# Kernel tuning notes

Hardware: AMD Instinct MI355X
Metric: run time of the kernel (lower is better)

## Reference

```python
import jax, jax.numpy as jnp
import numpy as np

NUM_HEADS = 4
EPS = 1e-5

def _proj(x, W, b):
    # 1x1x1 Conv3d == channel-wise linear: x [B,C,H,W,D], W [Cout,Cin], b [Cout]
    return jnp.einsum('oc,bchwd->bohwd', W, x) + b[None, :, None, None, None]

def setup_inputs() -> dict:
    key = jax.random.key(0)
    ks = jax.random.split(key, 12)
    B, C, H, W, D = 2, 128, 16, 16, 16
    s = 1.0 / np.sqrt(C)
    inp = {
        'query_features': jax.random.normal(ks[0], (B, C, H, W, D), jnp.float32),
        'key_value_features': jax.random.normal(ks[1], (B, C, H, W, D), jnp.float32),
        'Wq': jax.random.normal(ks[2], (C, C), jnp.float32) * s,
        'bq': jax.random.normal(ks[3], (C,), jnp.float32) * 0.01,
        'Wk': jax.random.normal(ks[4], (C, C), jnp.float32) * s,
        'bk': jax.random.normal(ks[5], (C,), jnp.float32) * 0.01,
        'Wv': jax.random.normal(ks[6], (C, C), jnp.float32) * s,
        'bv': jax.random.normal(ks[7], (C,), jnp.float32) * 0.01,
        'Wo': jax.random.normal(ks[8], (C, C), jnp.float32) * s,
        'bo': jax.random.normal(ks[9], (C,), jnp.float32) * 0.01,
    }
    return inp

def reference(query_features, key_value_features, Wq, bq, Wk, bk, Wv, bv, Wo, bo):
    B, C, H, W, D = query_features.shape
    hd = C // NUM_HEADS  # head_dim
    N = H * W * D
    Q = _proj(query_features, Wq, bq).reshape(B, NUM_HEADS, hd, N)
    K = _proj(key_value_features, Wk, bk).reshape(B, NUM_HEADS, hd, N)
    V = _proj(key_value_features, Wv, bv).reshape(B, NUM_HEADS, hd, N)
    scale = hd ** -0.5
    attn = jnp.einsum('bhdn,bhdm->bhnm', Q, K) * scale  # [B,h,N,N]
    attn = jax.nn.softmax(attn, axis=-1)
    out = jnp.einsum('bhnm,bhdm->bhdn', attn, V).reshape(B, C, H, W, D)
    out = _proj(out, Wo, bo)
    res = query_features + out
    # InstanceNorm3d (affine=False): normalize over spatial dims per (B,C)
    mu = jnp.mean(res, axis=(2, 3, 4), keepdims=True)
    var = jnp.var(res, axis=(2, 3, 4), keepdims=True)
    return (res - mu) * jax.lax.rsqrt(var + EPS)
```

## Files before the change

### kernel.cpp

```cpp
#include <hip/hip_runtime.h>
#include <hip/hip_bf16.h>

typedef unsigned short u16;
typedef unsigned int u32;
typedef __bf16 bf16_t;
typedef bf16_t bf16x8 __attribute__((ext_vector_type(8)));
typedef float f32x4 __attribute__((ext_vector_type(4)));

#define NTOT 4096
#define CCH 128
#define QSCL 0.25503486703f

__device__ __forceinline__ float bf2f(u16 x) {
    return __uint_as_float(((u32)x) << 16);
}
__device__ __forceinline__ u32 pkbf(float a, float b) {
    __hip_bfloat162 h = __float22bfloat162_rn(make_float2(a, b));
    u32 r; __builtin_memcpy(&r, &h, 4); return r;
}
__device__ __forceinline__ u16 f2bf(float a) {
    return (u16)(pkbf(a, a) & 0xffffu);
}

__global__ __launch_bounds__(256) void prep_kernel(
    const float* __restrict__ Wq, const float* __restrict__ Wk,
    const float* __restrict__ Wv, const float* __restrict__ Wo,
    const float* __restrict__ bq,
    u16* __restrict__ Wqb, u16* __restrict__ Wkb,
    u16* __restrict__ Wvb, u16* __restrict__ Wob,
    float* __restrict__ bqs)
{
    const int idx = blockIdx.x * 256 + threadIdx.x;
    const int m = idx >> 13;
    const int e = idx & 8191;
    const float* src = (m == 0) ? Wq : (m == 1) ? Wk : (m == 2) ? Wv : Wo;
    u32* dst = (u32*)((m == 0) ? Wqb : (m == 1) ? Wkb : (m == 2) ? Wvb : Wob);
    const float s = (m == 0) ? QSCL : 1.0f;
    float2 f = ((const float2*)src)[e];
    dst[e] = pkbf(f.x * s, f.y * s);
    if (idx < CCH) bqs[idx] = bq[idx] * QSCL;
}

__global__ __launch_bounds__(256, 4) void proj_kernel(
    const float* __restrict__ xq, const float* __restrict__ xkv,
    const u16* __restrict__ Wqb, const float* __restrict__ bqs,
    const u16* __restrict__ Wkb, const float* __restrict__ bk_,
    const u16* __restrict__ Wvb, const float* __restrict__ bv_,
    u16* __restrict__ Qt, u16* __restrict__ Kt, u16* __restrict__ Vn)
{
    const int nt = blockIdx.x, p = blockIdx.y, b = blockIdx.z;
    const float* X    = (p == 0) ? xq : xkv;
    const u16*   Wb   = (p == 0) ? Wqb : (p == 1) ? Wkb : Wvb;
    const float* bias = (p == 0) ? bqs : (p == 1) ? bk_ : bv_;
    const int n0 = nt * 64;
    const int tid = threadIdx.x;

    __shared__ u16 Xt[64 * 128];
    __shared__ u16 Wl[128 * 136];

    #pragma unroll
    for (int k = 0; k < 4; ++k) {
        int n = tid & 63;
        int c = (tid >> 6) + k * 4;
        float f[8];
        #pragma unroll
        for (int j = 0; j < 8; ++j)
            f[j] = X[((size_t)(b * CCH) + 8 * c + j) * NTOT + n0 + n];
        uint4 vv = {pkbf(f[0], f[1]), pkbf(f[2], f[3]), pkbf(f[4], f[5]), pkbf(f[6], f[7])};
        *(uint4*)(Xt + n * 128 + ((c ^ (n & 7)) * 8)) = vv;
    }
    #pragma unroll
    for (int k = 0; k < 8; ++k) {
        int id = tid + k * 256;
        int row = id >> 4;
        int off = (id & 15) * 8;
        *(uint4*)(Wl + row * 136 + off) = *(const uint4*)(Wb + row * 128 + off);
    }
    __syncthreads();

    const int wave = tid >> 6, lane = tid & 63;
    const int quad = lane >> 4, l16 = lane & 15;
    f32x4 acc[8];
    #pragma unroll
    for (int cf = 0; cf < 8; ++cf) acc[cf] = (f32x4){0.f, 0.f, 0.f, 0.f};

    #pragma unroll
    for (int kk = 0; kk < 4; ++kk) {
        bf16x8 bx = *(const bf16x8*)(Xt + (wave * 16 + l16) * 128 +
                                     (((kk * 4 + quad) ^ (l16 & 7)) * 8));
        #pragma unroll
        for (int cf = 0; cf < 8; ++cf) {
            bf16x8 aw = *(const bf16x8*)(Wl + (cf * 16 + l16) * 136 + kk * 32 + quad * 8);
            acc[cf] = __builtin_amdgcn_mfma_f32_16x16x32_bf16(aw, bx, acc[cf], 0, 0, 0);
        }
    }

    const int n = n0 + wave * 16 + l16;
    #pragma unroll
    for (int cf = 0; cf < 8; ++cf) {
        float4 b4 = *(const float4*)(bias + cf * 16 + quad * 4);
        float v0 = acc[cf][0] + b4.x;
        float v1 = acc[cf][1] + b4.y;
        float v2 = acc[cf][2] + b4.z;
        float v3 = acc[cf][3] + b4.w;
        if (p < 2) {
            const int h = cf >> 1;
            const int d0 = (cf & 1) * 16 + quad * 4;
            u16* dst = (p == 0 ? Qt : Kt) + ((size_t)(b * 4 + h) * NTOT + n) * 32 + d0;
            uint2 vv = {pkbf(v0, v1), pkbf(v2, v3)};
            *(uint2*)dst = vv;
        } else {
            int c = cf * 16 + quad * 4;
            u16* dst = Vn + (size_t)(b * CCH + c) * NTOT + n;
            dst[0 * NTOT] = f2bf(v0); dst[1 * NTOT] = f2bf(v1);
            dst[2 * NTOT] = f2bf(v2); dst[3 * NTOT] = f2bf(v3);
        }
    }
}

__global__ __launch_bounds__(256, 2) void flash_attn_kernel(
    const u16* __restrict__ Qt, const u16* __restrict__ Kt,
    const u16* __restrict__ Vn, u16* __restrict__ pO, float* __restrict__ pL)
{
    const int bh = blockIdx.z, kc = blockIdx.y;
    const int wave = threadIdx.x >> 6, lane = threadIdx.x & 63;
    const int q = lane >> 4, l16 = lane & 15;
    const int q0w = blockIdx.x * 256 + wave * 64;

    const u16* Qbh = Qt + (size_t)bh * NTOT * 32;
    const u16* Kbh = Kt + (size_t)bh * NTOT * 32;
    const u16* Vg  = Vn + ((size_t)((bh >> 2) * CCH + (bh & 3) * 32)) * NTOT;

    __shared__ u16 Kb[2][2048];
    __shared__ u16 Vb[2][2048];
    __shared__ u16 Pb[4][1024];

    const int kbase = kc * 1024;

    bf16x8 bq[4];
    #pragma unroll
    for (int g = 0; g < 4; ++g)
        bq[g] = *(const bf16x8*)(Qbh + (size_t)(q0w + g * 16 + l16) * 32 + q * 8);

    const size_t ksrc = (size_t)(wave * 16 + l16) * 32 + q * 8;
    const size_t vsrc = (size_t)((wave & 1) * 16 + l16) * NTOT + (wave >> 1) * 32 + q * 8;
    const int kv_dst = wave * 512 + lane * 8;

    uint4 kreg = *(const uint4*)(Kbh + (size_t)kbase * 32 + ksrc);
    uint4 vreg = *(const uint4*)(Vg + vsrc + kbase);
    *(uint4*)(&Kb[0][kv_dst]) = kreg;
    *(uint4*)(&Vb[0][kv_dst]) = vreg;
    __syncthreads();

    f32x4 o[4][2];
    #pragma unroll
    for (int g = 0; g < 4; ++g) {
        o[g][0] = (f32x4){0,0,0,0};
        o[g][1] = (f32x4){0,0,0,0};
    }
    const f32x4 zero = {0,0,0,0};
    float lp[4] = {0.f, 0.f, 0.f, 0.f};

    u16* pw = &Pb[wave][0];
    const int pwr = (q >> 1) * 128 + l16 * 8 + (q & 1) * 4;
    const int prd0 = 0 * 512 + lane * 8;
    const int prd1 = 1 * 512 + lane * 8;

    for (int it = 0; it < 16; ++it) {
        const int cur = it & 1;
        if (it < 15) {
            const int m1 = kbase + (it + 1) * 64;
            kreg = *(const uint4*)(Kbh + (size_t)m1 * 32 + ksrc);
            vreg = *(const uint4*)(Vg + vsrc + m1);
        }
        f32x4 s[4][4];
        #pragma unroll
        for (int t = 0; t < 4; ++t) {
            bf16x8 ak = *(const bf16x8*)(&Kb[cur][t * 512 + lane * 8]);
            #pragma unroll
            for (int g = 0; g < 4; ++g)
                s[g][t] = __builtin_amdgcn_mfma_f32_16x16x32_bf16(ak, bq[g], zero, 0, 0, 0);
        }
        bf16x8 av00 = *(const bf16x8*)(&Vb[cur][0 * 512 + lane * 8]);
        bf16x8 av01 = *(const bf16x8*)(&Vb[cur][1 * 512 + lane * 8]);
        bf16x8 av10 = *(const bf16x8*)(&Vb[cur][2 * 512 + lane * 8]);
        bf16x8 av11 = *(const bf16x8*)(&Vb[cur][3 * 512 + lane * 8]);
        #pragma unroll
        for (int g = 0; g < 4; ++g) {
            #pragma unroll
            for (int t = 0; t < 4; ++t) {
                float p0 = __builtin_amdgcn_exp2f(s[g][t][0]);
                float p1 = __builtin_amdgcn_exp2f(s[g][t][1]);
                float p2 = __builtin_amdgcn_exp2f(s[g][t][2]);
                float p3 = __builtin_amdgcn_exp2f(s[g][t][3]);
                lp[g] += (p0 + p1) + (p2 + p3);
                uint2 wv = {pkbf(p0, p1), pkbf(p2, p3)};
                *(uint2*)(pw + (t >> 1) * 512 + (t & 1) * 256 + pwr) = wv;
            }
            bf16x8 pb0 = *(const bf16x8*)(pw + prd0);
            bf16x8 pb1 = *(const bf16x8*)(pw + prd1);
            o[g][0] = __builtin_amdgcn_mfma_f32_16x16x32_bf16(av00, pb0, o[g][0], 0, 0, 0);
            o[g][1] = __builtin_amdgcn_mfma_f32_16x16x32_bf16(av01, pb0, o[g][1], 0, 0, 0);
            o[g][0] = __builtin_amdgcn_mfma_f32_16x16x32_bf16(av10, pb1, o[g][0], 0, 0, 0);
            o[g][1] = __builtin_amdgcn_mfma_f32_16x16x32_bf16(av11, pb1, o[g][1], 0, 0, 0);
        }
        if (it < 15) {
            const int nb = (it + 1) & 1;
            *(uint4*)(&Kb[nb][kv_dst]) = kreg;
            *(uint4*)(&Vb[nb][kv_dst]) = vreg;
        }
        __syncthreads();
    }

    #pragma unroll
    for (int g = 0; g < 4; ++g) {
        lp[g] += __shfl_xor(lp[g], 16);
        lp[g] += __shfl_xor(lp[g], 32);
        const size_t ob = ((size_t)(kc * 8 + bh) * NTOT + q0w + g * 16 + l16) * 32 + q * 4;
        uint2 w0 = {pkbf(o[g][0][0], o[g][0][1]), pkbf(o[g][0][2], o[g][0][3])};
        uint2 w1 = {pkbf(o[g][1][0], o[g][1][1]), pkbf(o[g][1][2], o[g][1][3])};
        *(uint2*)(pO + ob)      = w0;
        *(uint2*)(pO + ob + 16) = w1;
        if (q == 0)
            pL[(size_t)(kc * 8 + bh) * NTOT + q0w + g * 16 + l16] = lp[g];
    }
}

__global__ __launch_bounds__(256, 4) void outproj_kernel(
    const float* __restrict__ xq,
    const u16* __restrict__ pO, const float* __restrict__ pL,
    const u16* __restrict__ Wob, const float* __restrict__ bo,
    float* __restrict__ res, float* __restrict__ partS, float* __restrict__ partQ)
{
    const int nt = blockIdx.x, ct = blockIdx.y, b = blockIdx.z;
    const int n0 = nt * 64;
    const int tid = threadIdx.x;

    __shared__ u16 Xt[64 * 128];
    __shared__ u16 Wl[64 * 136];

    #pragma unroll
    for (int k = 0; k < 4; ++k) {
        int cid = tid + k * 256;
        int n = cid >> 4;
        int ch = cid & 15;
        int bh = b * 4 + (ch >> 2);
        int d0 = (ch & 3) * 8;
        float l = 0.f;
        float v[8];
        #pragma unroll
        for (int j = 0; j < 8; ++j) v[j] = 0.f;
        #pragma unroll
        for (int kcc = 0; kcc < 4; ++kcc) {
            const size_t nrow = (size_t)(kcc * 8 + bh) * NTOT + n0 + n;
            l += pL[nrow];
            uint4 u = *(const uint4*)(pO + nrow * 32 + d0);
            const u32 uu[4] = {u.x, u.y, u.z, u.w};
            #pragma unroll
            for (int j = 0; j < 4; ++j) {
                v[2 * j]     += bf2f((u16)(uu[j] & 0xffffu));
                v[2 * j + 1] += bf2f((u16)(uu[j] >> 16));
            }
        }
        const float inv = 1.0f / l;
        uint4 vv = {pkbf(v[0] * inv, v[1] * inv), pkbf(v[2] * inv, v[3] * inv),
                    pkbf(v[4] * inv, v[5] * inv), pkbf(v[6] * inv, v[7] * inv)};
        *(uint4*)(Xt + n * 128 + ((ch ^ (n & 7)) * 8)) = vv;
    }
    #pragma unroll
    for (int k = 0; k < 4; ++k) {
        int id = tid + k * 256;
        int row = id >> 4;
        int off = (id & 15) * 8;
        *(uint4*)(Wl + row * 136 + off) =
            *(const uint4*)(Wob + (size_t)(ct * 64 + row) * 128 + off);
    }
    __syncthreads();

    const int wave = tid >> 6, lane = tid & 63;
    const int quad = lane >> 4, l16 = lane & 15;
    f32x4 acc[4];
    #pragma unroll
    for (int cf = 0; cf < 4; ++cf) acc[cf] = (f32x4){0.f, 0.f, 0.f, 0.f};

    #pragma unroll
    for (int kk = 0; kk < 4; ++kk) {
        bf16x8 bx = *(const bf16x8*)(Xt + (wave * 16 + l16) * 128 +
                                     (((kk * 4 + quad) ^ (l16 & 7)) * 8));
        #pragma unroll
        for (int cf = 0; cf < 4; ++cf) {
            bf16x8 aw = *(const bf16x8*)(Wl + (cf * 16 + l16) * 136 + kk * 32 + quad * 8);
            acc[cf] = __builtin_amdgcn_mfma_f32_16x16x32_bf16(aw, bx, acc[cf], 0, 0, 0);
        }
    }

    const int n = n0 + wave * 16 + l16;
    const int tile = nt * 4 + wave;
    #pragma unroll
    for (int cf = 0; cf < 4; ++cf) {
        float4 b4 = *(const float4*)(bo + ct * 64 + cf * 16 + quad * 4);
        const float bb[4] = {b4.x, b4.y, b4.z, b4.w};
        float sv[4], qv[4];
        #pragma unroll
        for (int r = 0; r < 4; ++r) {
            int c = ct * 64 + cf * 16 + quad * 4 + r;
            float v = acc[cf][r] + bb[r] + xq[(size_t)(b * CCH + c) * NTOT + n];
            res[(size_t)(b * CCH + c) * NTOT + n] = v;
            sv[r] = v;
            qv[r] = v * v;
        }
        #pragma unroll
        for (int off = 1; off < 16; off <<= 1) {
            #pragma unroll
            for (int r = 0; r < 4; ++r) {
                sv[r] += __shfl_xor(sv[r], off);
                qv[r] += __shfl_xor(qv[r], off);
            }
        }
        if (l16 == 0) {
            #pragma unroll
            for (int r = 0; r < 4; ++r) {
                int c = ct * 64 + cf * 16 + quad * 4 + r;
                partS[(size_t)(b * CCH + c) * 256 + tile] = sv[r];
                partQ[(size_t)(b * CCH + c) * 256 + tile] = qv[r];
            }
        }
    }
}

__global__ __launch_bounds__(256) void norm_kernel(
    const float* __restrict__ res, const float* __restrict__ partS,
    const float* __restrict__ partQ, float* __restrict__ out)
{
    const int c = blockIdx.x, b = blockIdx.y;
    const int tid = threadIdx.x;
    const size_t row = (size_t)(b * CCH + c);
    __shared__ float rs[4], rq[4];
    float s = partS[row * 256 + tid];
    float q = partQ[row * 256 + tid];
    #pragma unroll
    for (int off = 1; off < 64; off <<= 1) {
        s += __shfl_xor(s, off);
        q += __shfl_xor(q, off);
    }
    const int wv = tid >> 6, ln = tid & 63;
    if (ln == 0) { rs[wv] = s; rq[wv] = q; }
    __syncthreads();
    float ts = rs[0] + rs[1] + rs[2] + rs[3];
    float tq = rq[0] + rq[1] + rq[2] + rq[3];
    float mu  = ts * (1.0f / 4096.0f);
    float var = tq * (1.0f / 4096.0f) - mu * mu;
    float inv = rsqrtf(var + 1e-5f);
    const size_t base = row * NTOT;
    #pragma unroll
    for (int j = 0; j < 4; ++j) {
        int n = tid * 4 + j * 1024;
        float4 v = *(const float4*)(res + base + n);
        float4 o;
        o.x = (v.x - mu) * inv; o.y = (v.y - mu) * inv;
        o.z = (v.z - mu) * inv; o.w = (v.w - mu) * inv;
        *(float4*)(out + base + n) = o;
    }
}

extern "C" void kernel_launch(void* const* d_in, const int* in_sizes, int n_in,
                              void* d_out, int out_size, void* d_ws, size_t ws_size,
                              hipStream_t stream)
{
    const float* xq  = (const float*)d_in[0];
    const float* xkv = (const float*)d_in[1];
    const float* Wq  = (const float*)d_in[2];
    const float* bq  = (const float*)d_in[3];
    const float* Wk  = (const float*)d_in[4];
    const float* bk  = (const float*)d_in[5];
    const float* Wv  = (const float*)d_in[6];
    const float* bv  = (const float*)d_in[7];
    const float* Wo  = (const float*)d_in[8];
    const float* bo  = (const float*)d_in[9];
    float* out = (float*)d_out;

    char* ws = (char*)d_ws;
    const size_t MB = (size_t)1 << 20;
    u16* Qt = (u16*)(ws + 0 * MB);
    u16* Kt = (u16*)(ws + 2 * MB);
    u16* Vn = (u16*)(ws + 4 * MB);
    u16* pO = (u16*)(ws + 6 * MB);
    float* pL = (float*)(ws + 14 * MB);
    u16* Wqb = (u16*)(ws + 15 * MB);
    u16* Wkb = Wqb + 16384;
    u16* Wvb = Wkb + 16384;
    u16* Wob = Wvb + 16384;
    float* bqs = (float*)(Wob + 16384);
    float* res   = (float*)(ws + 16 * MB);
    float* partS = (float*)(ws + 20 * MB);
    float* partQ = (float*)(ws + 20 * MB + 262144);

    prep_kernel<<<dim3(128), 256, 0, stream>>>(Wq, Wk, Wv, Wo, bq, Wqb, Wkb, Wvb, Wob, bqs);
    proj_kernel<<<dim3(64, 3, 2), 256, 0, stream>>>(xq, xkv, Wqb, bqs, Wkb, bk, Wvb, bv, Qt, Kt, Vn);
    flash_attn_kernel<<<dim3(16, 4, 8), 256, 0, stream>>>(Qt, Kt, Vn, pO, pL);
    outproj_kernel<<<dim3(64, 2, 2), 256, 0, stream>>>(xq, pO, pL, Wob, bo, res, partS, partQ);
    norm_kernel<<<dim3(128, 2), 256, 0, stream>>>(res, partS, partQ, out);
}
```

Baseline: 126.9 us.

## Fold weight prep into projections and fuse norm via grid barrier

Drops the separate weight-conversion kernel: proj and outproj now read fp32 weights and convert them to bf16 in-kernel, folding the Q scale into the conversion. The instance-norm kernel is merged into outproj through a global atomic counter barrier, reset by flash_attn, so each of the 256 blocks waits for all partial sums and then normalizes one (b,c) row. This removes two launches but adds redundant weight conversion per block. It also relies on all 256 blocks being co-resident; the spin loop is bounded, so an unmet barrier would read incomplete partials rather than hang.

```diff
diff --git a/kernel.cpp b/kernel.cpp
--- a/kernel.cpp
+++ b/kernel.cpp
@@ -22,36 +22,18 @@
     return (u16)(pkbf(a, a) & 0xffffu);
 }
 
-__global__ __launch_bounds__(256) void prep_kernel(
-    const float* __restrict__ Wq, const float* __restrict__ Wk,
-    const float* __restrict__ Wv, const float* __restrict__ Wo,
-    const float* __restrict__ bq,
-    u16* __restrict__ Wqb, u16* __restrict__ Wkb,
-    u16* __restrict__ Wvb, u16* __restrict__ Wob,
-    float* __restrict__ bqs)
-{
-    const int idx = blockIdx.x * 256 + threadIdx.x;
-    const int m = idx >> 13;
-    const int e = idx & 8191;
-    const float* src = (m == 0) ? Wq : (m == 1) ? Wk : (m == 2) ? Wv : Wo;
-    u32* dst = (u32*)((m == 0) ? Wqb : (m == 1) ? Wkb : (m == 2) ? Wvb : Wob);
-    const float s = (m == 0) ? QSCL : 1.0f;
-    float2 f = ((const float2*)src)[e];
-    dst[e] = pkbf(f.x * s, f.y * s);
-    if (idx < CCH) bqs[idx] = bq[idx] * QSCL;
-}
-
 __global__ __launch_bounds__(256, 4) void proj_kernel(
     const float* __restrict__ xq, const float* __restrict__ xkv,
-    const u16* __restrict__ Wqb, const float* __restrict__ bqs,
-    const u16* __restrict__ Wkb, const float* __restrict__ bk_,
-    const u16* __restrict__ Wvb, const float* __restrict__ bv_,
+    const float* __restrict__ Wq, const float* __restrict__ bq,
+    const float* __restrict__ Wk, const float* __restrict__ bk_,
+    const float* __restrict__ Wv, const float* __restrict__ bv_,
     u16* __restrict__ Qt, u16* __restrict__ Kt, u16* __restrict__ Vn)
 {
     const int nt = blockIdx.x, p = blockIdx.y, b = blockIdx.z;
     const float* X    = (p == 0) ? xq : xkv;
-    const u16*   Wb   = (p == 0) ? Wqb : (p == 1) ? Wkb : Wvb;
-    const float* bias = (p == 0) ? bqs : (p == 1) ? bk_ : bv_;
+    const float* Wf   = (p == 0) ? Wq : (p == 1) ? Wk : Wv;
+    const float* bias = (p == 0) ? bq : (p == 1) ? bk_ : bv_;
+    const float s = (p == 0) ? QSCL : 1.0f;
     const int n0 = nt * 64;
     const int tid = threadIdx.x;
 
@@ -74,7 +56,12 @@
         int id = tid + k * 256;
         int row = id >> 4;
         int off = (id & 15) * 8;
-        *(uint4*)(Wl + row * 136 + off) = *(const uint4*)(Wb + row * 128 + off);
+        const float* wsrc = Wf + row * 128 + off;
+        float4 wa = *(const float4*)(wsrc);
+        float4 wc = *(const float4*)(wsrc + 4);
+        uint4 vv = {pkbf(wa.x * s, wa.y * s), pkbf(wa.z * s, wa.w * s),
+                    pkbf(wc.x * s, wc.y * s), pkbf(wc.z * s, wc.w * s)};
+        *(uint4*)(Wl + row * 136 + off) = vv;
     }
     __syncthreads();
 
@@ -99,10 +86,10 @@
     #pragma unroll
     for (int cf = 0; cf < 8; ++cf) {
         float4 b4 = *(const float4*)(bias + cf * 16 + quad * 4);
-        float v0 = acc[cf][0] + b4.x;
-        float v1 = acc[cf][1] + b4.y;
-        float v2 = acc[cf][2] + b4.z;
-        float v3 = acc[cf][3] + b4.w;
+        float v0 = acc[cf][0] + b4.x * s;
+        float v1 = acc[cf][1] + b4.y * s;
+        float v2 = acc[cf][2] + b4.z * s;
+        float v3 = acc[cf][3] + b4.w * s;
         if (p < 2) {
             const int h = cf >> 1;
             const int d0 = (cf & 1) * 16 + quad * 4;
@@ -120,8 +107,12 @@
 
 __global__ __launch_bounds__(256, 2) void flash_attn_kernel(
     const u16* __restrict__ Qt, const u16* __restrict__ Kt,
-    const u16* __restrict__ Vn, u16* __restrict__ pO, float* __restrict__ pL)
+    const u16* __restrict__ Vn, u16* __restrict__ pO, float* __restrict__ pL,
+    u32* __restrict__ counter)
 {
+    if ((blockIdx.x | blockIdx.y | blockIdx.z | threadIdx.x) == 0)
+        __hip_atomic_store(counter, 0u, __ATOMIC_RELAXED, __HIP_MEMORY_SCOPE_AGENT);
+
     const int bh = blockIdx.z, kc = blockIdx.y;
     const int wave = threadIdx.x >> 6, lane = threadIdx.x & 63;
     const int q = lane >> 4, l16 = lane & 15;
@@ -229,8 +220,9 @@
 __global__ __launch_bounds__(256, 4) void outproj_kernel(
     const float* __restrict__ xq,
     const u16* __restrict__ pO, const float* __restrict__ pL,
-    const u16* __restrict__ Wob, const float* __restrict__ bo,
-    float* __restrict__ res, float* __restrict__ partS, float* __restrict__ partQ)
+    const float* __restrict__ Wo, const float* __restrict__ bo,
+    float* __restrict__ res, float* __restrict__ partS, float* __restrict__ partQ,
+    float* __restrict__ out, u32* __restrict__ counter)
 {
     const int nt = blockIdx.x, ct = blockIdx.y, b = blockIdx.z;
     const int n0 = nt * 64;
@@ -238,6 +230,7 @@
 
     __shared__ u16 Xt[64 * 128];
     __shared__ u16 Wl[64 * 136];
+    __shared__ float rs[4], rq[4];
 
     #pragma unroll
     for (int k = 0; k < 4; ++k) {
@@ -272,8 +265,12 @@
         int id = tid + k * 256;
         int row = id >> 4;
         int off = (id & 15) * 8;
-        *(uint4*)(Wl + row * 136 + off) =
-            *(const uint4*)(Wob + (size_t)(ct * 64 + row) * 128 + off);
+        const float* wsrc = Wo + (size_t)(ct * 64 + row) * 128 + off;
+        float4 wa = *(const float4*)(wsrc);
+        float4 wc = *(const float4*)(wsrc + 4);
+        uint4 vv = {pkbf(wa.x, wa.y), pkbf(wa.z, wa.w),
+                    pkbf(wc.x, wc.y), pkbf(wc.z, wc.w)};
+        *(uint4*)(Wl + row * 136 + off) = vv;
     }
     __syncthreads();
 
@@ -326,25 +323,29 @@
             }
         }
     }
-}
-
-__global__ __launch_bounds__(256) void norm_kernel(
-    const float* __restrict__ res, const float* __restrict__ partS,
-    const float* __restrict__ partQ, float* __restrict__ out)
-{
-    const int c = blockIdx.x, b = blockIdx.y;
-    const int tid = threadIdx.x;
-    const size_t row = (size_t)(b * CCH + c);
-    __shared__ float rs[4], rq[4];
-    float s = partS[row * 256 + tid];
-    float q = partQ[row * 256 + tid];
-    #pragma unroll
-    for (int off = 1; off < 64; off <<= 1) {
-        s += __shfl_xor(s, off);
-        q += __shfl_xor(q, off);
-    }
-    const int wv = tid >> 6, ln = tid & 63;
-    if (ln == 0) { rs[wv] = s; rq[wv] = q; }
+
+    __threadfence();
+    __syncthreads();
+    if (tid == 0) {
+        __hip_atomic_fetch_add(counter, 1u, __ATOMIC_ACQ_REL, __HIP_MEMORY_SCOPE_AGENT);
+        for (int i = 0; i < (1 << 21); ++i) {
+            if (__hip_atomic_load(counter, __ATOMIC_ACQUIRE, __HIP_MEMORY_SCOPE_AGENT) >= 256u)
+                break;
+            __builtin_amdgcn_s_sleep(2);
+        }
+    }
+    __syncthreads();
+
+    const int rowid = blockIdx.x + 64 * (blockIdx.y + 2 * blockIdx.z);
+    const size_t row = (size_t)rowid;
+    float s2 = partS[row * 256 + tid];
+    float q2 = partQ[row * 256 + tid];
+    #pragma unroll
+    for (int off2 = 1; off2 < 64; off2 <<= 1) {
+        s2 += __shfl_xor(s2, off2);
+        q2 += __shfl_xor(q2, off2);
+    }
+    if (lane == 0) { rs[wave] = s2; rq[wave] = q2; }
     __syncthreads();
     float ts = rs[0] + rs[1] + rs[2] + rs[3];
     float tq = rq[0] + rq[1] + rq[2] + rq[3];
@@ -354,12 +355,12 @@
     const size_t base = row * NTOT;
     #pragma unroll
     for (int j = 0; j < 4; ++j) {
-        int n = tid * 4 + j * 1024;
-        float4 v = *(const float4*)(res + base + n);
+        int nn = tid * 4 + j * 1024;
+        float4 v = *(const float4*)(res + base + nn);
         float4 o;
         o.x = (v.x - mu) * inv; o.y = (v.y - mu) * inv;
         o.z = (v.z - mu) * inv; o.w = (v.w - mu) * inv;
-        *(float4*)(out + base + n) = o;
+        *(float4*)(out + base + nn) = o;
     }
 }
 
@@ -386,18 +387,12 @@
     u16* Vn = (u16*)(ws + 4 * MB);
     u16* pO = (u16*)(ws + 6 * MB);
     float* pL = (float*)(ws + 14 * MB);
-    u16* Wqb = (u16*)(ws + 15 * MB);
-    u16* Wkb = Wqb + 16384;
-    u16* Wvb = Wkb + 16384;
-    u16* Wob = Wvb + 16384;
-    float* bqs = (float*)(Wob + 16384);
     float* res   = (float*)(ws + 16 * MB);
     float* partS = (float*)(ws + 20 * MB);
     float* partQ = (float*)(ws + 20 * MB + 262144);
-
-    prep_kernel<<<dim3(128), 256, 0, stream>>>(Wq, Wk, Wv, Wo, bq, Wqb, Wkb, Wvb, Wob, bqs);
-    proj_kernel<<<dim3(64, 3, 2), 256, 0, stream>>>(xq, xkv, Wqb, bqs, Wkb, bk, Wvb, bv, Qt, Kt, Vn);
-    flash_attn_kernel<<<dim3(16, 4, 8), 256, 0, stream>>>(Qt, Kt, Vn, pO, pL);
-    outproj_kernel<<<dim3(64, 2, 2), 256, 0, stream>>>(xq, pO, pL, Wob, bo, res, partS, partQ);
-    norm_kernel<<<dim3(128, 2), 256, 0, stream>>>(res, partS, partQ, out);
-}
+    u32* cnt = (u32*)(ws + 21 * MB);
+
+    proj_kernel<<<dim3(64, 3, 2), 256, 0, stream>>>(xq, xkv, Wq, bq, Wk, bk, Wv, bv, Qt, Kt, Vn);
+    flash_attn_kernel<<<dim3(16, 4, 8), 256, 0, stream>>>(Qt, Kt, Vn, pO, pL, cnt);
+    outproj_kernel<<<dim3(64, 2, 2), 256, 0, stream>>>(xq, pO, pL, Wo, bo, res, partS, partQ, out, cnt);
+}
```

Result: slower. 169.5 us (+33.6%).
